# Performance work log

Measured on AMD Instinct MI355X. Metric: run time of the kernel, lower is better.

## Reference

```python
import jax, jax.numpy as jnp
import numpy as np
from jax import lax

VOCAB = 10000
HID = 512
BATCH = 128
SEQ = 64
SCALE = 0.1


def setup_inputs() -> dict:
    key = jax.random.key(0)
    ks = jax.random.split(key, 16)
    u = lambda k, shape: jax.random.uniform(k, shape, jnp.float32, -SCALE, SCALE)
    return {
        "features": jax.random.randint(ks[0], (BATCH, SEQ), 0, VOCAB, jnp.int32),
        "labels": jax.random.randint(ks[1], (BATCH, SEQ), 0, VOCAB, jnp.int32),
        "seq_lengths": jax.random.randint(ks[2], (BATCH,), 0, SEQ, jnp.int32),
        "seq_mask": jax.random.uniform(ks[3], (BATCH, SEQ), jnp.float32),
        "embedding": u(ks[4], (VOCAB, HID)),
        "W0x": u(ks[5], (HID, 4 * HID)),
        "W0h": u(ks[6], (HID, 4 * HID)),
        "b0": jnp.zeros((4 * HID,), jnp.float32),
        "W1x": u(ks[7], (HID, 4 * HID)),
        "W1h": u(ks[8], (HID, 4 * HID)),
        "b1": jnp.zeros((4 * HID,), jnp.float32),
        "softmax_w": u(ks[9], (HID, VOCAB)),
        "softmax_b": jnp.zeros((VOCAB,), jnp.float32),
    }


def _lstm_cell(h, c, xin, Wx, Wh, b, m):
    # forget_bias = 0.0 (as in LSTMBlockCell(forget_bias=0.0))
    g = xin @ Wx + h @ Wh + b            # [B, 4H]
    i, cg, f, o = jnp.split(g, 4, axis=-1)
    c_new = jax.nn.sigmoid(f) * c + jax.nn.sigmoid(i) * jnp.tanh(cg)
    h_new = jax.nn.sigmoid(o) * jnp.tanh(c_new)
    # sequence_length masking: freeze state, zero output past length
    return m * h_new + (1 - m) * h, m * c_new + (1 - m) * c, m * h_new


def reference(features, labels, seq_lengths, seq_mask, embedding,
              W0x, W0h, b0, W1x, W1h, b1, softmax_w, softmax_b):
    x = embedding[features]                       # [B, T, H]
    B, T, H = x.shape
    xs = jnp.swapaxes(x, 0, 1)                    # [T, B, H]
    act = (jnp.arange(T)[:, None] < seq_lengths[None, :]).astype(x.dtype)[..., None]  # [T,B,1]

    def step(carry, inp):
        h0, c0, h1, c1 = carry
        xt, m = inp
        h0, c0, o0 = _lstm_cell(h0, c0, xt, W0x, W0h, b0, m)
        h1, c1, o1 = _lstm_cell(h1, c1, o0, W1x, W1h, b1, m)
        return (h0, c0, h1, c1), o1

    init = tuple(jnp.zeros((B, H), x.dtype) for _ in range(4))
    _, outs = lax.scan(step, init, (xs, act))     # [T, B, H]
    out = jnp.swapaxes(outs, 0, 1)                # [B, T, H]

    logits = out @ softmax_w + softmax_b          # [B, T, V]
    logp = jax.nn.log_softmax(logits, axis=-1)
    xent = -jnp.take_along_axis(logp, labels[..., None], axis=-1)[..., 0]  # [B, T]
    # tf.contrib.seq2seq.sequence_loss(average_across_batch=True, average_across_timesteps=False)
    loss_t = jnp.sum(xent * seq_mask, axis=0) / (jnp.sum(seq_mask, axis=0) + 1e-12)  # [T]
    cost = jnp.mean(loss_t)
    return cost
```

## Files before the change

### kernel.cpp

```cpp
#include <hip/hip_runtime.h>
#include <hip/hip_bf16.h>

#define BB 128
#define TT 64
#define HH 512
#define VV 10000
#define VP 10048
#define NTILES 157
#define NCHUNK 16
#define TPC 10
#define NBLK 256

typedef __attribute__((ext_vector_type(8))) __bf16 bf16x8;
typedef __attribute__((ext_vector_type(4))) float f32x4;
typedef unsigned short ushort_t;

__device__ __forceinline__ ushort_t f2bf(float x) {
  union { float f; unsigned u; } v; v.f = x;
  unsigned r = v.u + 0x7fffu + ((v.u >> 16) & 1u);
  return (ushort_t)(r >> 16);
}

__device__ __forceinline__ f32x4 mfma16(bf16x8 a, bf16x8 b, f32x4 c) {
  return __builtin_amdgcn_mfma_f32_16x16x32_bf16(a, b, c, 0, 0, 0);
}

__device__ __forceinline__ float fsig(float x) {
  return __builtin_amdgcn_rcpf(1.f + __expf(-x));
}
__device__ __forceinline__ float ftanh(float x) {
  return 1.f - 2.f * __builtin_amdgcn_rcpf(__expf(2.f * x) + 1.f);
}

__device__ __forceinline__ bf16x8 load16_sc1(const ushort_t* p) {
  bf16x8 r;
  asm volatile("global_load_dwordx4 %0, %1, off sc1" : "=v"(r) : "v"(p) : "memory");
  return r;
}

__device__ __forceinline__ void store16B_sc1(ushort_t* p, bf16x8 v) {
  asm volatile("global_store_dwordx4 %0, %1, off sc1" :: "v"(p), "v"(v) : "memory");
}

__device__ __forceinline__ void glds16(const ushort_t* g, ushort_t* l) {
  __builtin_amdgcn_global_load_lds(
      (const __attribute__((address_space(1))) unsigned*)g,
      (__attribute__((address_space(3))) unsigned*)l, 16, 0, 0);
}

__global__ void k_trans_w(const float* __restrict__ Wx0, const float* __restrict__ Wh0,
                          const float* __restrict__ Wx1, const float* __restrict__ Wh1,
                          ushort_t* __restrict__ dst0, ushort_t* __restrict__ dst1) {
  __shared__ float tile[64][65];
  const int kt = blockIdx.x * 64;
  const int ct = blockIdx.y * 64;
  const float* Wx = blockIdx.z ? Wx1 : Wx0;
  const float* Wh = blockIdx.z ? Wh1 : Wh0;
  ushort_t* dst = blockIdx.z ? dst1 : dst0;
  const int tid = threadIdx.x;
  const int cl = tid & 63;
  const int cp = ct + cl;
  const int col = (cp & 3) * 512 + (cp >> 2);
#pragma unroll
  for (int r = 0; r < 16; ++r) {
    const int kl = r * 4 + (tid >> 6);
    const int k = kt + kl;
    tile[cl][kl] = (k < 512) ? Wx[k * 2048 + col] : Wh[(k - 512) * 2048 + col];
  }
  __syncthreads();
#pragma unroll
  for (int s = 0; s < 16; ++s) {
    const int idx = tid + s * 256;
    const int cl2 = idx >> 6, kl2 = idx & 63;
    dst[(size_t)(ct + cl2) * 1024 + kt + kl2] = f2bf(tile[cl2][kl2]);
  }
}

__global__ void k_trans_sw(const float* __restrict__ sw, ushort_t* __restrict__ dst) {
  __shared__ float tile[64][65];
  const int kt = blockIdx.x * 64;
  const int vt = blockIdx.y * 64;
  const int tid = threadIdx.x;
  const int vl = tid & 63;
  const int v = vt + vl;
#pragma unroll
  for (int r = 0; r < 16; ++r) {
    const int kl = r * 4 + (tid >> 6);
    tile[vl][kl] = (v < VV) ? sw[(size_t)(kt + kl) * VV + v] : 0.f;
  }
  __syncthreads();
#pragma unroll
  for (int s = 0; s < 16; ++s) {
    const int idx = tid + s * 256;
    const int vl2 = idx >> 6, kl2 = idx & 63;
    const int k = kt + kl2;
    const int kb = k >> 3;
    const int kp = (((kb ^ (vl2 & 7)) << 3) | (k & 7));
    dst[(size_t)(vt + vl2) * 512 + kp] = f2bf(tile[vl2][kl2]);
  }
}

__global__ void k_misc(const int* __restrict__ feat, const float* __restrict__ emb,
                       ushort_t* __restrict__ xb, ushort_t* __restrict__ h0,
                       ushort_t* __restrict__ h1, unsigned* __restrict__ bar) {
  const int stride = gridDim.x * blockDim.x;
  for (int e = blockIdx.x * blockDim.x + threadIdx.x; e < 8192 * 512; e += stride) {
    const int row = e >> 9;
    const int t = row >> 7, b = row & 127;
    const int f = feat[b * 64 + t];
    xb[e] = f2bf(emb[(size_t)f * 512 + (e & 511)]);
    if (e < 2 * 128 * 512) { h0[e] = 0; h1[e] = 0; }
    if (e < 512) bar[e] = 0u;
  }
}

__global__ __launch_bounds__(256, 1) void k_scan(
    const ushort_t* __restrict__ xb, const ushort_t* __restrict__ W0t,
    const ushort_t* __restrict__ W1t, const float* __restrict__ b0,
    const float* __restrict__ b1, ushort_t* __restrict__ h0g,
    ushort_t* __restrict__ h1g, ushort_t* __restrict__ out1,
    const int* __restrict__ seqlen, unsigned* __restrict__ bar) {
  __shared__ ushort_t act[32 * 128 * 8];
  __shared__ ushort_t hst[32][16];
  __shared__ ushort_t ost[32][16];
  __shared__ int sl_sh[32];
  const int bid = blockIdx.x;
  const int layer = bid >> 7;
  const int lb = bid & 127;
  const int cblk = lb >> 2;
  const int bquad = lb & 3;
  const int grp = bid & 3;
  const int tid = threadIdx.x;
  const int w = tid >> 6;
  const int lane = tid & 63;
  const int fr = lane & 15;
  const int hi = lane >> 4;
  const int w4hi = w * 4 + hi;

  const ushort_t* Wt = layer ? W1t : W0t;
  const float* bias = layer ? b1 : b0;
  ushort_t* hbuf = layer ? h1g : h0g;

  if (tid < 32) sl_sh[tid] = seqlen[bquad * 32 + tid];

  bf16x8 wreg[32];
  {
    const ushort_t* wp = Wt + (size_t)(cblk * 64 + w * 16 + fr) * 1024 + hi * 8;
#pragma unroll
    for (int ks = 0; ks < 32; ++ks)
      wreg[ks] = *reinterpret_cast<const bf16x8*>(wp + ks * 32);
  }

  const int u = cblk * 16 + w4hi;
  const float bi = bias[u];
  const float bc = bias[512 + u];
  const float bf_ = bias[1024 + u];
  const float bo = bias[1536 + u];

  __syncthreads();
  const int sl0 = sl_sh[fr];
  const int sl1 = sl_sh[fr + 16];

  float c0s = 0.f, c1s = 0.f;
  float h0s = 0.f, h1s = 0.f;

#pragma unroll 1
  for (int p = 0; p <= 64; ++p) {
    const int t = layer ? (p - 1) : p;
    const bool active = layer ? (p >= 1) : (p < 64);

    asm volatile("s_waitcnt vmcnt(0)" ::: "memory");
    __syncthreads();
    if (tid == 0) {
      const unsigned old = __hip_atomic_fetch_add(&bar[grp * 16], 1u,
                                                  __ATOMIC_RELAXED, __HIP_MEMORY_SCOPE_AGENT);
      if (old + 1 == 64u * (unsigned)(p + 1))
        __hip_atomic_store(&bar[256 + grp * 16], (unsigned)(p + 1), __ATOMIC_RELAXED,
                           __HIP_MEMORY_SCOPE_AGENT);
    }
    if (layer == 0 && active) {
      const ushort_t* xsrc = xb + (size_t)t * 128 * 512;
#pragma unroll
      for (int i = 0; i < 8; ++i) {
        const int idx = i * 256 + tid;
        const int b = idx >> 6;
        const int kp = idx & 63;
        const int kslot = (kp & 0x30) | ((kp & 15) ^ (b & 15));
        const ushort_t* s = xsrc + (size_t)(bquad * 32 + b) * 512 + (kslot << 3);
        *reinterpret_cast<bf16x8*>(&act[(b * 128 + kp) * 8]) =
            *reinterpret_cast<const bf16x8*>(s);
      }
    }
    if (tid == 0) {
      while (__hip_atomic_load(&bar[256 + grp * 16], __ATOMIC_RELAXED,
                               __HIP_MEMORY_SCOPE_AGENT) < (unsigned)(p + 1))
        __builtin_amdgcn_s_sleep(1);
    }
    __syncthreads();

    if (active) {
      if (layer == 1) {
        bf16x8 tmp[16];
        const ushort_t* xsrc = h0g + (size_t)(p & 1) * 128 * 512;
        const ushort_t* hsrc = h1g + (size_t)(t & 1) * 128 * 512;
        int dsts[16];
#pragma unroll
        for (int i = 0; i < 8; ++i) {
          const int idx = i * 256 + tid;
          const int b = idx >> 6;
          const int kp = idx & 63;
          const int kslot = (kp & 0x30) | ((kp & 15) ^ (b & 15));
          tmp[i] = load16_sc1(xsrc + (size_t)(bquad * 32 + b) * 512 + (kslot << 3));
          dsts[i] = (b * 128 + kp) * 8;
        }
#pragma unroll
        for (int i = 0; i < 8; ++i) {
          const int idx = i * 256 + tid;
          const int b = idx >> 6;
          const int kp = 64 + (idx & 63);
          const int kslot = (kp & 0x70) | ((kp & 15) ^ (b & 15));
          tmp[8 + i] = load16_sc1(hsrc + (size_t)(bquad * 32 + b) * 512 + ((kslot - 64) << 3));
          dsts[8 + i] = (b * 128 + kp) * 8;
        }
        asm volatile("s_waitcnt vmcnt(0)" ::: "memory");
        __builtin_amdgcn_sched_barrier(0);
        const bf16x8 ZV = {};
#pragma unroll
        for (int i = 0; i < 8; ++i) {
          const int b = (i * 256 + tid) >> 6;
          *reinterpret_cast<bf16x8*>(&act[dsts[i]]) = (t < sl_sh[b]) ? tmp[i] : ZV;
        }
#pragma unroll
        for (int i = 0; i < 8; ++i)
          *reinterpret_cast<bf16x8*>(&act[dsts[8 + i]]) = tmp[8 + i];
      } else {
        bf16x8 tmp[8];
        const ushort_t* hsrc = h0g + (size_t)(t & 1) * 128 * 512;
        int dsts[8];
#pragma unroll
        for (int i = 0; i < 8; ++i) {
          const int idx = i * 256 + tid;
          const int b = idx >> 6;
          const int kp = 64 + (idx & 63);
          const int kslot = (kp & 0x70) | ((kp & 15) ^ (b & 15));
          tmp[i] = load16_sc1(hsrc + (size_t)(bquad * 32 + b) * 512 + ((kslot - 64) << 3));
          dsts[i] = (b * 128 + kp) * 8;
        }
        asm volatile("s_waitcnt vmcnt(0)" ::: "memory");
        __builtin_amdgcn_sched_barrier(0);
#pragma unroll
        for (int i = 0; i < 8; ++i)
          *reinterpret_cast<bf16x8*>(&act[dsts[i]]) = tmp[i];
      }
      __syncthreads();

      f32x4 acc0 = (f32x4){0.f, 0.f, 0.f, 0.f};
      f32x4 acc1 = (f32x4){0.f, 0.f, 0.f, 0.f};
#pragma unroll
      for (int ks = 0; ks < 32; ++ks) {
        const int kslot = ks * 4 + hi;
        const int kp = (kslot & 0x70) | ((kslot & 15) ^ fr);
        const bf16x8 bf0 = *reinterpret_cast<const bf16x8*>(&act[(fr * 128 + kp) * 8]);
        const bf16x8 bf1 = *reinterpret_cast<const bf16x8*>(&act[((16 + fr) * 128 + kp) * 8]);
        acc0 = mfma16(wreg[ks], bf0, acc0);
        acc1 = mfma16(wreg[ks], bf1, acc1);
      }
      __syncthreads();

      {
        const float si = fsig(acc0[0] + bi);
        const float tc = ftanh(acc0[1] + bc);
        const float sf = fsig(acc0[2] + bf_);
        const float so = fsig(acc0[3] + bo);
        const float cn = sf * c0s + si * tc;
        const float hn = so * ftanh(cn);
        const bool msk = t < sl0;
        if (msk) { c0s = cn; h0s = hn; }
        hst[fr][w4hi] = f2bf(h0s);
        if (layer) ost[fr][w4hi] = msk ? f2bf(hn) : (ushort_t)0;
      }
      {
        const float si = fsig(acc1[0] + bi);
        const float tc = ftanh(acc1[1] + bc);
        const float sf = fsig(acc1[2] + bf_);
        const float so = fsig(acc1[3] + bo);
        const float cn = sf * c1s + si * tc;
        const float hn = so * ftanh(cn);
        const bool msk = t < sl1;
        if (msk) { c1s = cn; h1s = hn; }
        hst[fr + 16][w4hi] = f2bf(h1s);
        if (layer) ost[fr + 16][w4hi] = msk ? f2bf(hn) : (ushort_t)0;
      }
      __syncthreads();

      if (tid < 64) {
        const int bl = tid >> 1, hf = tid & 1;
        const size_t off = (size_t)(bquad * 32 + bl) * 512 + cblk * 16 + hf * 8;
        ushort_t* hp = hbuf + (size_t)((t + 1) & 1) * 128 * 512 + off;
        const bf16x8 hv = *reinterpret_cast<const bf16x8*>(&hst[bl][hf * 8]);
        store16B_sc1(hp, hv);
        if (layer) {
          const bf16x8 ovv = *reinterpret_cast<const bf16x8*>(&ost[bl][hf * 8]);
          *reinterpret_cast<bf16x8*>(out1 + (size_t)t * 128 * 512 + off) = ovv;
        }
      }
    }
  }
}

__global__ __launch_bounds__(256, 2) void k_loss_gemm(
    const ushort_t* __restrict__ A, const ushort_t* __restrict__ SWTs,
    const float* __restrict__ sb, const int* __restrict__ labels,
    float* __restrict__ part) {
  __shared__ ushort_t Bl[2][32 * 512];
  __shared__ float sbl[640];
  const int tid = threadIdx.x;
  const int lane = tid & 63;
  const int w = tid >> 6;
  const int fr = lane & 15;
  const int fk = (lane >> 4) << 3;
  const int rowbase = blockIdx.x * 128 + w * 32;
  const int chunk = blockIdx.y;
  const int tile_lo = chunk * TPC;
  const int tile_hi = (tile_lo + TPC < NTILES) ? (tile_lo + TPC) : NTILES;
  const int nhalf = (tile_hi - tile_lo) * 2;

  for (int i = tid; i < 640; i += 256) {
    const int v = chunk * 640 + i;
    sbl[i] = (v < VV) ? sb[v] : 0.f;
  }

  bf16x8 a[2][16];
#pragma unroll
  for (int rf = 0; rf < 2; ++rf) {
    const ushort_t* ap = A + (size_t)(rowbase + rf * 16 + fr) * 512 + fk;
#pragma unroll
    for (int ks = 0; ks < 16; ++ks) a[rf][ks] = *reinterpret_cast<const bf16x8*>(ap + ks * 32);
  }

  int lab[2][4];
  float m[2][4], l[2][4], ll[2][4];
#pragma unroll
  for (int rf = 0; rf < 2; ++rf)
#pragma unroll
    for (int r = 0; r < 4; ++r) {
      const int rg = rowbase + rf * 16 + ((lane >> 4) << 2) + r;
      lab[rf][r] = labels[(rg & 127) * 64 + (rg >> 7)];
      m[rf][r] = -3.0e38f; l[rf][r] = 0.f; ll[rf][r] = 0.f;
    }
  __syncthreads();

#define STAGE(BUF, HIDX)                                                         \
  do {                                                                           \
    const size_t gbase = (size_t)(tile_lo * 2 + (HIDX)) * 32 * 512;              \
    _Pragma("unroll")                                                            \
    for (int i_ = 0; i_ < 8; ++i_) {                                             \
      glds16(SWTs + gbase + (size_t)(i_ * 256 + tid) * 8,                        \
             &Bl[BUF][i_ * 2048 + w * 512]);                                     \
    }                                                                            \
  } while (0)

  f32x4 acc[2][4];
  STAGE(0, 0);

#pragma unroll 1
  for (int idx = 0; idx < nhalf; ++idx) {
    const int cur = idx & 1;
    if (idx + 1 < nhalf) {
      STAGE(cur ^ 1, idx + 1);
      asm volatile("s_waitcnt vmcnt(8)" ::: "memory");
    } else {
      asm volatile("s_waitcnt vmcnt(0)" ::: "memory");
    }
    __builtin_amdgcn_s_barrier();
    __builtin_amdgcn_sched_barrier(0);

    if ((idx & 1) == 0) {
      acc[0][0] = (f32x4){0.f,0.f,0.f,0.f}; acc[0][1] = (f32x4){0.f,0.f,0.f,0.f};
      acc[1][0] = (f32x4){0.f,0.f,0.f,0.f}; acc[1][1] = (f32x4){0.f,0.f,0.f,0.f};
#pragma unroll
      for (int ks = 0; ks < 16; ++ks) {
#pragma unroll
        for (int j = 0; j < 2; ++j) {
          const int vloc = j * 16 + fr;
          const int kb = ks * 4 + (fk >> 3);
          const bf16x8 b = *reinterpret_cast<const bf16x8*>(
              &Bl[cur][vloc * 512 + ((kb ^ (vloc & 7)) << 3)]);
          acc[0][j] = mfma16(a[0][ks], b, acc[0][j]);
          acc[1][j] = mfma16(a[1][ks], b, acc[1][j]);
        }
      }
    } else {
      acc[0][2] = (f32x4){0.f,0.f,0.f,0.f}; acc[0][3] = (f32x4){0.f,0.f,0.f,0.f};
      acc[1][2] = (f32x4){0.f,0.f,0.f,0.f}; acc[1][3] = (f32x4){0.f,0.f,0.f,0.f};
#pragma unroll
      for (int ks = 0; ks < 16; ++ks) {
#pragma unroll
        for (int j = 0; j < 2; ++j) {
          const int vloc = j * 16 + fr;
          const int kb = ks * 4 + (fk >> 3);
          const bf16x8 b = *reinterpret_cast<const bf16x8*>(
              &Bl[cur][vloc * 512 + ((kb ^ (vloc & 7)) << 3)]);
          acc[0][2 + j] = mfma16(a[0][ks], b, acc[0][2 + j]);
          acc[1][2 + j] = mfma16(a[1][ks], b, acc[1][2 + j]);
        }
      }

      const int tl = idx >> 1;
      const int vb = (tile_lo + tl) * 64;
      float sbt[4]; bool vld[4];
#pragma unroll
      for (int cf = 0; cf < 4; ++cf) {
        const int v = vb + cf * 16 + fr;
        vld[cf] = v < VV;
        sbt[cf] = sbl[tl * 64 + cf * 16 + fr];
      }
#pragma unroll
      for (int rf = 0; rf < 2; ++rf)
#pragma unroll
        for (int r = 0; r < 4; ++r) {
          const float x0 = vld[0] ? acc[rf][0][r] + sbt[0] : -3.0e38f;
          const float x1 = vld[1] ? acc[rf][1][r] + sbt[1] : -3.0e38f;
          const float x2 = vld[2] ? acc[rf][2][r] + sbt[2] : -3.0e38f;
          const float x3 = vld[3] ? acc[rf][3][r] + sbt[3] : -3.0e38f;
          const float tm = fmaxf(fmaxf(x0, x1), fmaxf(x2, x3));
          if (tm > -1.0e37f) {
            const float mn = fmaxf(m[rf][r], tm);
            const float sc = __expf(m[rf][r] - mn);
            const float se = __expf(x0 - mn) + __expf(x1 - mn) +
                             __expf(x2 - mn) + __expf(x3 - mn);
            l[rf][r] = l[rf][r] * sc + se;
            m[rf][r] = mn;
          }
          const int lt = lab[rf][r] - vb;
          if (lt >= 0 && lt < 64 && fr == (lt & 15)) {
            const int cf = lt >> 4;
            ll[rf][r] += (cf == 0) ? x0 : (cf == 1) ? x1 : (cf == 2) ? x2 : x3;
          }
        }
    }
    __builtin_amdgcn_s_barrier();
  }
#undef STAGE

#pragma unroll
  for (int rf = 0; rf < 2; ++rf)
#pragma unroll
    for (int r = 0; r < 4; ++r) {
      float mm = m[rf][r], lv = l[rf][r], lv2 = ll[rf][r];
#pragma unroll
      for (int sh = 1; sh < 16; sh <<= 1) {
        const float m2 = __shfl_xor(mm, sh, 64);
        const float l2 = __shfl_xor(lv, sh, 64);
        const float ll2 = __shfl_xor(lv2, sh, 64);
        const float mn = fmaxf(mm, m2);
        lv = lv * __expf(mm - mn) + l2 * __expf(m2 - mn);
        mm = mn;
        lv2 += ll2;
      }
      if (fr == 0) {
        const int rg = rowbase + rf * 16 + ((lane >> 4) << 2) + r;
        float* p = part + ((size_t)chunk * 8192 + rg) * 4;
        p[0] = mm; p[1] = lv; p[2] = lv2;
      }
    }
}

__global__ void k_loss_merge(const float* __restrict__ part, float* __restrict__ xent) {
  const int row = blockIdx.x * 256 + threadIdx.x;
  float m = -3.0e38f, l = 0.f, ll = 0.f;
#pragma unroll
  for (int c = 0; c < NCHUNK; ++c) {
    const float* p = part + ((size_t)c * 8192 + row) * 4;
    const float pm = p[0], pl = p[1], pll = p[2];
    const float mn = fmaxf(m, pm);
    l = l * __expf(m - mn) + pl * __expf(pm - mn);
    m = mn;
    ll += pll;
  }
  xent[row] = m + logf(l) - ll;
}

__global__ void k_final(const float* __restrict__ xent, const float* __restrict__ mask,
                        float* __restrict__ out) {
  __shared__ float partial[4];
  const int lane = threadIdx.x & 63;
  const int w = threadIdx.x >> 6;
  float accT = 0.f;
  for (int i = 0; i < 16; ++i) {
    const int t = w * 16 + i;
    const float m1 = mask[lane * 64 + t];
    const float m2 = mask[(lane + 64) * 64 + t];
    float s = xent[t * 128 + lane] * m1 + xent[t * 128 + lane + 64] * m2;
    float sm = m1 + m2;
#pragma unroll
    for (int sh = 1; sh < 64; sh <<= 1) {
      s += __shfl_xor(s, sh, 64);
      sm += __shfl_xor(sm, sh, 64);
    }
    accT += s / (sm + 1e-12f);
  }
  if (lane == 0) partial[w] = accT;
  __syncthreads();
  if (threadIdx.x == 0)
    out[0] = (partial[0] + partial[1] + partial[2] + partial[3]) * (1.f / 64.f);
}

extern "C" void kernel_launch(void* const* d_in, const int* in_sizes, int n_in,
                              void* d_out, int out_size, void* d_ws, size_t ws_size,
                              hipStream_t stream) {
  const int* feat = (const int*)d_in[0];
  const int* labels = (const int*)d_in[1];
  const int* seqlen = (const int*)d_in[2];
  const float* seqmask = (const float*)d_in[3];
  const float* emb = (const float*)d_in[4];
  const float* W0x = (const float*)d_in[5];
  const float* W0h = (const float*)d_in[6];
  const float* b0 = (const float*)d_in[7];
  const float* W1x = (const float*)d_in[8];
  const float* W1h = (const float*)d_in[9];
  const float* b1 = (const float*)d_in[10];
  const float* sw = (const float*)d_in[11];
  const float* sbv = (const float*)d_in[12];

  ushort_t* W0t = (ushort_t*)d_ws;
  ushort_t* W1t = W0t + (size_t)2048 * 1024;
  ushort_t* SWT = W1t + (size_t)2048 * 1024;
  ushort_t* xb = SWT + (size_t)VP * 512;
  ushort_t* out1 = xb + (size_t)8192 * 512;
  ushort_t* h0g = out1 + (size_t)8192 * 512;
  ushort_t* h1g = h0g + (size_t)2 * 128 * 512;
  float* xent = (float*)(h1g + (size_t)2 * 128 * 512);
  float* part = xent + 8192;
  unsigned* bar = (unsigned*)(part + (size_t)NCHUNK * 8192 * 4);

  k_trans_w<<<dim3(16, 32, 2), 256, 0, stream>>>(W0x, W0h, W1x, W1h, W0t, W1t);
  k_trans_sw<<<dim3(8, 157), 256, 0, stream>>>(sw, SWT);
  k_misc<<<4096, 256, 0, stream>>>(feat, emb, xb, h0g, h1g, bar);

  {
    const ushort_t* a0 = xb; const ushort_t* a1 = W0t; const ushort_t* a2 = W1t;
    const float* a3 = b0; const float* a4 = b1;
    ushort_t* a5 = h0g; ushort_t* a6 = h1g; ushort_t* a7 = out1;
    const int* a8 = seqlen; unsigned* a9 = bar;
    void* args[] = {(void*)&a0, (void*)&a1, (void*)&a2, (void*)&a3, (void*)&a4,
                    (void*)&a5, (void*)&a6, (void*)&a7, (void*)&a8, (void*)&a9};
    hipLaunchCooperativeKernel((const void*)k_scan, dim3(NBLK), dim3(256), args, 0, stream);
  }

  k_loss_gemm<<<dim3(64, NCHUNK), 256, 0, stream>>>(out1, SWT, sbv, labels, part);
  k_loss_merge<<<32, 256, 0, stream>>>(part, xent);
  k_final<<<1, 256, 0, stream>>>(xent, seqmask, (float*)d_out);
}
```

Before: 475.1 us.

## Overlap layer-0 input projection with grid barrier wait; remap loss GEMM grid

In the recurrent scan, layer-0 blocks now run the x-dependent half of the gate MFMA (k-slots 0-15) before spinning on the inter-block barrier. After the barrier they only load h and finish the remaining 16 k-slots. This moves input-projection work off the critical serial path between timesteps, at the cost of an extra __syncthreads. Separately, the loss GEMM launch is flattened to a 1D grid with the vocab chunk as the fast index, so consecutive blocks share rows of A and spread across different softmax-weight chunks, which changes cache locality.

Result: faster. 464.5 us (-2.2%).

```diff
diff --git a/kernel.cpp b/kernel.cpp
--- a/kernel.cpp
+++ b/kernel.cpp
@@ -168,14 +168,18 @@
   for (int p = 0; p <= 64; ++p) {
     const int t = layer ? (p - 1) : p;
     const bool active = layer ? (p >= 1) : (p < 64);
+    const unsigned target = (unsigned)(p + 1);
+
+    f32x4 acc0 = (f32x4){0.f, 0.f, 0.f, 0.f};
+    f32x4 acc1 = (f32x4){0.f, 0.f, 0.f, 0.f};
 
     asm volatile("s_waitcnt vmcnt(0)" ::: "memory");
     __syncthreads();
     if (tid == 0) {
       const unsigned old = __hip_atomic_fetch_add(&bar[grp * 16], 1u,
                                                   __ATOMIC_RELAXED, __HIP_MEMORY_SCOPE_AGENT);
-      if (old + 1 == 64u * (unsigned)(p + 1))
-        __hip_atomic_store(&bar[256 + grp * 16], (unsigned)(p + 1), __ATOMIC_RELAXED,
+      if (old + 1 == 64u * target)
+        __hip_atomic_store(&bar[256 + grp * 16], target, __ATOMIC_RELAXED,
                            __HIP_MEMORY_SCOPE_AGENT);
     }
     if (layer == 0 && active) {
@@ -190,10 +194,20 @@
         *reinterpret_cast<bf16x8*>(&act[(b * 128 + kp) * 8]) =
             *reinterpret_cast<const bf16x8*>(s);
       }
+      __syncthreads();
+#pragma unroll
+      for (int ks = 0; ks < 16; ++ks) {
+        const int kslot = ks * 4 + hi;
+        const int kp = (kslot & 0x70) | ((kslot & 15) ^ fr);
+        const bf16x8 bf0 = *reinterpret_cast<const bf16x8*>(&act[(fr * 128 + kp) * 8]);
+        const bf16x8 bf1 = *reinterpret_cast<const bf16x8*>(&act[((16 + fr) * 128 + kp) * 8]);
+        acc0 = mfma16(wreg[ks], bf0, acc0);
+        acc1 = mfma16(wreg[ks], bf1, acc1);
+      }
     }
     if (tid == 0) {
       while (__hip_atomic_load(&bar[256 + grp * 16], __ATOMIC_RELAXED,
-                               __HIP_MEMORY_SCOPE_AGENT) < (unsigned)(p + 1))
+                               __HIP_MEMORY_SCOPE_AGENT) < target)
         __builtin_amdgcn_s_sleep(1);
     }
     __syncthreads();
@@ -233,6 +247,16 @@
 #pragma unroll
         for (int i = 0; i < 8; ++i)
           *reinterpret_cast<bf16x8*>(&act[dsts[8 + i]]) = tmp[8 + i];
+        __syncthreads();
+#pragma unroll
+        for (int ks = 0; ks < 32; ++ks) {
+          const int kslot = ks * 4 + hi;
+          const int kp = (kslot & 0x70) | ((kslot & 15) ^ fr);
+          const bf16x8 bf0 = *reinterpret_cast<const bf16x8*>(&act[(fr * 128 + kp) * 8]);
+          const bf16x8 bf1 = *reinterpret_cast<const bf16x8*>(&act[((16 + fr) * 128 + kp) * 8]);
+          acc0 = mfma16(wreg[ks], bf0, acc0);
+          acc1 = mfma16(wreg[ks], bf1, acc1);
+        }
       } else {
         bf16x8 tmp[8];
         const ushort_t* hsrc = h0g + (size_t)(t & 1) * 128 * 512;
@@ -251,19 +275,16 @@
 #pragma unroll
         for (int i = 0; i < 8; ++i)
           *reinterpret_cast<bf16x8*>(&act[dsts[i]]) = tmp[i];
-      }
-      __syncthreads();
-
-      f32x4 acc0 = (f32x4){0.f, 0.f, 0.f, 0.f};
-      f32x4 acc1 = (f32x4){0.f, 0.f, 0.f, 0.f};
-#pragma unroll
-      for (int ks = 0; ks < 32; ++ks) {
-        const int kslot = ks * 4 + hi;
-        const int kp = (kslot & 0x70) | ((kslot & 15) ^ fr);
-        const bf16x8 bf0 = *reinterpret_cast<const bf16x8*>(&act[(fr * 128 + kp) * 8]);
-        const bf16x8 bf1 = *reinterpret_cast<const bf16x8*>(&act[((16 + fr) * 128 + kp) * 8]);
-        acc0 = mfma16(wreg[ks], bf0, acc0);
-        acc1 = mfma16(wreg[ks], bf1, acc1);
+        __syncthreads();
+#pragma unroll
+        for (int ks = 16; ks < 32; ++ks) {
+          const int kslot = ks * 4 + hi;
+          const int kp = (kslot & 0x70) | ((kslot & 15) ^ fr);
+          const bf16x8 bf0 = *reinterpret_cast<const bf16x8*>(&act[(fr * 128 + kp) * 8]);
+          const bf16x8 bf1 = *reinterpret_cast<const bf16x8*>(&act[((16 + fr) * 128 + kp) * 8]);
+          acc0 = mfma16(wreg[ks], bf0, acc0);
+          acc1 = mfma16(wreg[ks], bf1, acc1);
+        }
       }
       __syncthreads();
 
@@ -319,8 +340,8 @@
   const int w = tid >> 6;
   const int fr = lane & 15;
   const int fk = (lane >> 4) << 3;
-  const int rowbase = blockIdx.x * 128 + w * 32;
-  const int chunk = blockIdx.y;
+  const int chunk = blockIdx.x & 15;
+  const int rowbase = (blockIdx.x >> 4) * 128 + w * 32;
   const int tile_lo = chunk * TPC;
   const int tile_hi = (tile_lo + TPC < NTILES) ? (tile_lo + TPC) : NTILES;
   const int nhalf = (tile_hi - tile_lo) * 2;
@@ -548,7 +569,7 @@
     hipLaunchCooperativeKernel((const void*)k_scan, dim3(NBLK), dim3(256), args, 0, stream);
   }
 
-  k_loss_gemm<<<dim3(64, NCHUNK), 256, 0, stream>>>(out1, SWT, sbv, labels, part);
+  k_loss_gemm<<<dim3(1024), 256, 0, stream>>>(out1, SWT, sbv, labels, part);
   k_loss_merge<<<32, 256, 0, stream>>>(part, xent);
   k_final<<<1, 256, 0, stream>>>(xent, seqmask, (float*)d_out);
 }
```
